# Kernel optimization log

Hardware: AMD Instinct MI355X
Metric: run time of the kernel (lower is better)

## Reference

```python
import jax, jax.numpy as jnp
import numpy as np

N_TYPES = 4
AEV_DIM = 384
HIDDEN = [160, 128, 96]
CELU_ALPHA = 0.1


def _init_params(key):
    dims = [AEV_DIM] + HIDDEN + [1]
    params = {}
    for li in range(len(dims) - 1):
        key, kw = jax.random.split(key)
        scale = 1.0 / np.sqrt(dims[li])
        # stacked over the N_TYPES per-atom-type experts
        params[f"W{li}"] = (jax.random.normal(kw, (N_TYPES, dims[li], dims[li + 1]), dtype=jnp.float32) * scale)
        params[f"b{li}"] = jnp.zeros((N_TYPES, dims[li + 1]), dtype=jnp.float32)
    return params


def setup_inputs() -> dict:
    key = jax.random.key(0)
    k1, k2, k3 = jax.random.split(key, 3)
    B, A = 2048, 64
    species = jax.random.randint(k1, (B, A), 0, N_TYPES, dtype=jnp.int64)
    aev = jax.random.normal(k2, (B, A, AEV_DIM), dtype=jnp.float32)
    inp = {"species": species, "aev": aev}
    inp.update(_init_params(k3))
    return inp


def _mlp(x, t, W0, b0, W1, b1, W2, b2, W3, b3):
    # x: [N, aev_dim] -> [N] per-atom energy for atom type t
    h = jax.nn.celu(x @ W0[t] + b0[t], alpha=CELU_ALPHA)
    h = jax.nn.celu(h @ W1[t] + b1[t], alpha=CELU_ALPHA)
    h = jax.nn.celu(h @ W2[t] + b2[t], alpha=CELU_ALPHA)
    return (h @ W3[t] + b3[t]).reshape(-1)


def reference(species, aev, W0, b0, W1, b1, W2, b2, W3, b3):
    B, A = species.shape
    sp = species.reshape(-1)            # [B*A]
    x = aev.reshape(-1, aev.shape[-1])  # [B*A, aev_dim]
    out = jnp.zeros(sp.shape, dtype=aev.dtype)  # padding_fill = 0
    for t in range(N_TYPES):  # fixed small expert set
        y = _mlp(x, t, W0, b0, W1, b1, W2, b2, W3, b3)
        out = jnp.where(sp == t, y, out)
    energies = out.reshape(B, A).sum(axis=1)  # reduce over atoms
    return species, energies
```

## Files before the change

kernel.cpp:

```cpp
#include <hip/hip_runtime.h>
#include <math.h>


#define NATOMS   131072
#define NMOL     2048
#define AEV      384
#define NTYPES   4
#define MBLK     64
#define PADTOT   (NATOMS + NTYPES * MBLK)
#define NBLK_MLP (PADTOT / MBLK)
#define NBLK_H   512

#define WB_L1 61440
#define WB_L2 81920
#define WB_T  94208

typedef __attribute__((ext_vector_type(8))) short bf16x8;
typedef __attribute__((ext_vector_type(4))) float f32x4;

__device__ __forceinline__ float celu01(float v) {
  return (v > 0.f) ? v : 0.1f * (__expf(v * 10.f) - 1.f);
}
__device__ __forceinline__ unsigned short f2bf(float x) {
  unsigned u = __float_as_uint(x);
  return (unsigned short)((u + 0x7FFFu + ((u >> 16) & 1u)) >> 16);
}
__device__ __forceinline__ float bf2f(unsigned short h) {
  return __uint_as_float(((unsigned)h) << 16);
}


__global__ void k_pre(const int* __restrict__ species, float* __restrict__ out,
                      int* __restrict__ perm, int* __restrict__ hist,
                      const float* __restrict__ W0, const float* __restrict__ W1,
                      const float* __restrict__ W2, unsigned short* __restrict__ WB) {
  const int tid = threadIdx.x, blk = blockIdx.x;
  const int i = blk * 256 + tid;
  perm[i] = -1;
  if (i < NATOMS) out[i] = (float)species[i];
  if (i < NMOL) out[NATOMS + i] = 0.f;

  for (int f = i; f < NTYPES * WB_T; f += PADTOT) {
    const int t = f / WB_T, e0 = f - t * WB_T;
    int base, NT, N;
    const float* W;
    if (e0 < WB_L1)      { base = 0;     NT = 10; N = 160; W = W0 + (size_t)t * AEV * 160; }
    else if (e0 < WB_L2) { base = WB_L1; NT = 8;  N = 128; W = W1 + (size_t)t * 160 * 128; }
    else                 { base = WB_L2; NT = 6;  N = 96;  W = W2 + (size_t)t * 128 * 96; }
    const int e = e0 - base, frag = e >> 9, r = e & 511, lane = r >> 3, j = r & 7;
    const int kt = frag / NT, nt = frag - kt * NT;
    const int k = kt * 32 + ((lane >> 4) << 3) + j, n = nt * 16 + (lane & 15);
    WB[(size_t)t * WB_T + e0] = f2bf(W[k * N + n]);
  }

  if (blk < NBLK_H) {
    const int sp = species[i];
    const int wv = tid >> 6;
    __shared__ int wc[4 * NTYPES];
#pragma unroll
    for (int t = 0; t < NTYPES; ++t) {
      const unsigned long long m = __ballot(sp == t);
      if ((tid & 63) == 0) wc[wv * NTYPES + t] = __popcll(m);
    }
    __syncthreads();
    if (tid < NTYPES)
      hist[tid * NBLK_H + blk] = wc[tid] + wc[4 + tid] + wc[8 + tid] + wc[12 + tid];
  }
}


__global__ void k_scan(const int* __restrict__ hist, int* __restrict__ poff,
                       int* __restrict__ boff) {
  __shared__ int tot[NTYPES], base[NTYPES];
  const int tid = threadIdx.x, wv = tid >> 6, lane = tid & 63;
  int s = 0;
  for (int c = 0; c < 8; ++c) s += hist[wv * NBLK_H + c * 64 + lane];
  for (int off = 32; off; off >>= 1) s += __shfl_down(s, off);
  if (lane == 0) tot[wv] = s;
  __syncthreads();
  if (tid == 0) {
    int acc = 0; poff[0] = 0;
    for (int t = 0; t < NTYPES; ++t) {
      base[t] = acc;
      acc += ((tot[t] + 63) >> 6) << 6;
      poff[t + 1] = acc;
    }
  }
  __syncthreads();
  int carry = base[wv];
  for (int c = 0; c < 8; ++c) {
    const int orig = hist[wv * NBLK_H + c * 64 + lane];
    int v = orig;
    for (int off = 1; off < 64; off <<= 1) {
      const int u = __shfl_up(v, off);
      if (lane >= off) v += u;
    }
    boff[wv * NBLK_H + c * 64 + lane] = carry + v - orig;
    carry += __shfl(v, 63);
  }
}

__global__ void k_scatter(const int* __restrict__ species, const int* __restrict__ boff,
                          int* __restrict__ perm) {
  const int tid = threadIdx.x, blk = blockIdx.x;
  const int i = blk * 256 + tid;
  const int sp = species[i];
  const int wv = tid >> 6;
  __shared__ int wc[4 * NTYPES];
  unsigned long long msel = 0;
#pragma unroll
  for (int t = 0; t < NTYPES; ++t) {
    const unsigned long long m = __ballot(sp == t);
    if ((tid & 63) == 0) wc[wv * NTYPES + t] = __popcll(m);
    if (sp == t) msel = m;
  }
  __syncthreads();
  int woff = 0;
  for (int w = 0; w < wv; ++w) woff += wc[w * NTYPES + sp];
  const int rk = __builtin_amdgcn_mbcnt_hi((unsigned)(msel >> 32),
                 __builtin_amdgcn_mbcnt_lo((unsigned)msel, 0));
  perm[boff[sp * NBLK_H + blk] + woff + rk] = i;
}


__global__ __launch_bounds__(256, 6) void k_mlp(
    const float* __restrict__ aev, const unsigned short* __restrict__ WB,
    const float* __restrict__ b0, const float* __restrict__ b1,
    const float* __restrict__ b2, const float* __restrict__ b3,
    const float* __restrict__ W3,
    const int* __restrict__ poff, const int* __restrict__ perm,
    float* __restrict__ outE)
{
  __shared__ __align__(16) unsigned short ARENA[64 * 168];
  __shared__ float red[256];
  __shared__ int   permS[64];

  const int tid  = threadIdx.x;
  const int lane = tid & 63;
  const int wv   = __builtin_amdgcn_readfirstlane(tid >> 6);
  const int quad = lane >> 4, l15 = lane & 15;
  const int slot0 = blockIdx.x * MBLK;

  if (tid < 64) permS[tid] = perm[slot0 + tid];
  int t_ = (slot0 >= poff[1]) + (slot0 >= poff[2]) + (slot0 >= poff[3]);
  if (t_ > 3) t_ = 3;
  const int t = __builtin_amdgcn_readfirstlane(t_);
  __syncthreads();

  const bf16x8* wb0 = (const bf16x8*)(WB + (size_t)t * WB_T);
  const bf16x8* wb1 = (const bf16x8*)(WB + (size_t)t * WB_T + WB_L1);
  const bf16x8* wb2 = (const bf16x8*)(WB + (size_t)t * WB_T + WB_L2);

  f32x4 acc0[10];
#pragma unroll
  for (int nt = 0; nt < 10; ++nt) {
    const float b = b0[t * 160 + nt * 16 + l15];
    acc0[nt] = (f32x4){b, b, b, b};
  }
  const int sm = tid >> 2, scg = tid & 3;
  const int sai = permS[sm];
  const float4* src = (const float4*)(aev + (size_t)(sai < 0 ? 0 : sai) * AEV);
  for (int s = 0; s < 4; ++s) {
#pragma unroll
    for (int ii = 0; ii < 6; ++ii) {
      const int c4 = scg + ii * 4;
      float4 v = make_float4(0.f, 0.f, 0.f, 0.f);
      if (sai >= 0) v = src[s * 24 + c4];
      ushort4 p = {f2bf(v.x), f2bf(v.y), f2bf(v.z), f2bf(v.w)};
      *(ushort4*)&ARENA[sm * 104 + c4 * 4] = p;
    }
    __syncthreads();
    const int arow = (wv * 16 + l15) * 104 + quad * 8;
#pragma unroll
    for (int ks = 0; ks < 3; ++ks) {
      const bf16x8 a = *(const bf16x8*)&ARENA[arow + ks * 32];
      const int ksg = s * 3 + ks;
#pragma unroll
      for (int nt = 0; nt < 10; ++nt)
        acc0[nt] = __builtin_amdgcn_mfma_f32_16x16x32_bf16(a, wb0[(ksg * 10 + nt) * 64 + lane], acc0[nt], 0, 0, 0);
    }
    __syncthreads();
  }
  {
    const int hrow0 = wv * 16 + quad * 4;
#pragma unroll
    for (int nt = 0; nt < 10; ++nt)
#pragma unroll
      for (int r = 0; r < 4; ++r)
        ARENA[(hrow0 + r) * 168 + nt * 16 + l15] = f2bf(celu01(acc0[nt][r]));
  }
  __syncthreads();

  f32x4 acc1[8];
#pragma unroll
  for (int nt = 0; nt < 8; ++nt) {
    const float b = b1[t * 128 + nt * 16 + l15];
    acc1[nt] = (f32x4){b, b, b, b};
  }
  {
    const int arow = (wv * 16 + l15) * 168 + quad * 8;
#pragma unroll
    for (int ks = 0; ks < 5; ++ks) {
      const bf16x8 a = *(const bf16x8*)&ARENA[arow + ks * 32];
#pragma unroll
      for (int nt = 0; nt < 8; ++nt)
        acc1[nt] = __builtin_amdgcn_mfma_f32_16x16x32_bf16(a, wb1[(ks * 8 + nt) * 64 + lane], acc1[nt], 0, 0, 0);
    }
  }
  __syncthreads();
  {
    const int hrow0 = wv * 16 + quad * 4;
#pragma unroll
    for (int nt = 0; nt < 8; ++nt)
#pragma unroll
      for (int r = 0; r < 4; ++r)
        ARENA[(hrow0 + r) * 136 + nt * 16 + l15] = f2bf(celu01(acc1[nt][r]));
  }
  __syncthreads();

  f32x4 acc2[6];
#pragma unroll
  for (int nt = 0; nt < 6; ++nt) {
    const float b = b2[t * 96 + nt * 16 + l15];
    acc2[nt] = (f32x4){b, b, b, b};
  }
  {
    const int arow = (wv * 16 + l15) * 136 + quad * 8;
#pragma unroll
    for (int ks = 0; ks < 4; ++ks) {
      const bf16x8 a = *(const bf16x8*)&ARENA[arow + ks * 32];
#pragma unroll
      for (int nt = 0; nt < 6; ++nt)
        acc2[nt] = __builtin_amdgcn_mfma_f32_16x16x32_bf16(a, wb2[(ks * 6 + nt) * 64 + lane], acc2[nt], 0, 0, 0);
    }
  }
  __syncthreads();
  {
    const int hrow0 = wv * 16 + quad * 4;
#pragma unroll
    for (int nt = 0; nt < 6; ++nt)
#pragma unroll
      for (int r = 0; r < 4; ++r)
        ARENA[(hrow0 + r) * 104 + nt * 16 + l15] = f2bf(celu01(acc2[nt][r]));
  }
  __syncthreads();

  const float* w3 = W3 + t * 96;
  float part = 0.f;
#pragma unroll
  for (int q = 0; q < 24; ++q) {
    const int c = wv * 24 + q;
    part = fmaf(bf2f(ARENA[lane * 104 + c]), w3[c], part);
  }
  red[wv * 64 + lane] = part;
  __syncthreads();
  if (wv == 0) {
    const float e = red[lane] + red[64 + lane] + red[128 + lane] + red[192 + lane] + b3[t];
    const int ai = permS[lane];
    if (ai >= 0) atomicAdd(&outE[ai >> 6], e);
  }
}


extern "C" void kernel_launch(void* const* d_in, const int* in_sizes, int n_in,
                              void* d_out, int out_size, void* d_ws, size_t ws_size,
                              hipStream_t stream)
{
  const int*   species = (const int*)d_in[0];
  const float* aev     = (const float*)d_in[1];
  const float* W0 = (const float*)d_in[2];
  const float* b0 = (const float*)d_in[3];
  const float* W1 = (const float*)d_in[4];
  const float* b1 = (const float*)d_in[5];
  const float* W2 = (const float*)d_in[6];
  const float* b2 = (const float*)d_in[7];
  const float* W3 = (const float*)d_in[8];
  const float* b3 = (const float*)d_in[9];
  float* out = (float*)d_out;

  int* poff = (int*)d_ws;
  int* hist = poff + 8;
  int* boff = hist + NTYPES * NBLK_H;
  int* perm = boff + NTYPES * NBLK_H;
  unsigned short* WB = (unsigned short*)(perm + PADTOT);

  k_pre    <<<PADTOT / 256, 256, 0, stream>>>(species, out, perm, hist, W0, W1, W2, WB);
  k_scan   <<<1, 256, 0, stream>>>(hist, poff, boff);
  k_scatter<<<NBLK_H, 256, 0, stream>>>(species, boff, perm);
  k_mlp    <<<NBLK_MLP, 256, 0, stream>>>(aev, WB, b0, b1, b2, b3, W3,
                                          poff, perm, out + NATOMS);
}
```

Before: 384.3 us.

## Use 2-wave blocks with two M-tiles per wave, direct AEV loads, MFMA final layer

Shrinks the MLP block to 128 threads, with each wave handling two 16-row tiles. Each weight fragment loaded from global is now reused across two MFMAs, halving weight traffic per row. The AEV input is read straight from global into registers in the MFMA A-fragment layout with software prefetch, replacing the LDS staging loop and its barriers. The last 96->1 layer becomes an MFMA instead of a scalar dot product plus LDS reduction. The cost is more accumulator registers per thread and a bf16 rounding of W3.

```diff
diff --git a/kernel.cpp b/kernel.cpp
--- a/kernel.cpp
+++ b/kernel.cpp
@@ -25,8 +25,11 @@
   unsigned u = __float_as_uint(x);
   return (unsigned short)((u + 0x7FFFu + ((u >> 16) & 1u)) >> 16);
 }
-__device__ __forceinline__ float bf2f(unsigned short h) {
-  return __uint_as_float(((unsigned)h) << 16);
+__device__ __forceinline__ unsigned int pk2(float lo, float hi) {
+  unsigned a = __float_as_uint(lo), b = __float_as_uint(hi);
+  a = (a + 0x7FFFu + ((a >> 16) & 1u)) >> 16;
+  b = ((b + 0x7FFFu + ((b >> 16) & 1u)) >> 16) << 16;
+  return a | b;
 }
 
 
@@ -123,7 +126,7 @@
 }
 
 
-__global__ __launch_bounds__(256, 6) void k_mlp(
+__global__ __launch_bounds__(128) void k_mlp(
     const float* __restrict__ aev, const unsigned short* __restrict__ WB,
     const float* __restrict__ b0, const float* __restrict__ b1,
     const float* __restrict__ b2, const float* __restrict__ b3,
@@ -131,9 +134,8 @@
     const int* __restrict__ poff, const int* __restrict__ perm,
     float* __restrict__ outE)
 {
-  __shared__ __align__(16) unsigned short ARENA[64 * 168];
-  __shared__ float red[256];
-  __shared__ int   permS[64];
+  __shared__ __align__(16) unsigned short H[64 * 168];
+  __shared__ int permS[64];
 
   const int tid  = threadIdx.x;
   const int lane = tid & 63;
@@ -147,118 +149,164 @@
   const int t = __builtin_amdgcn_readfirstlane(t_);
   __syncthreads();
 
+  const float* rp[2];
+#pragma unroll
+  for (int mtl = 0; mtl < 2; ++mtl) {
+    const int ai = permS[(2 * wv + mtl) * 16 + l15];
+    rp[mtl] = aev + (size_t)(ai < 0 ? 0 : ai) * AEV + quad * 8;
+  }
+
   const bf16x8* wb0 = (const bf16x8*)(WB + (size_t)t * WB_T);
   const bf16x8* wb1 = (const bf16x8*)(WB + (size_t)t * WB_T + WB_L1);
   const bf16x8* wb2 = (const bf16x8*)(WB + (size_t)t * WB_T + WB_L2);
 
-  f32x4 acc0[10];
+  union U8 { unsigned int u[4]; bf16x8 v; };
+
+  f32x4 acc0[10][2];
 #pragma unroll
   for (int nt = 0; nt < 10; ++nt) {
     const float b = b0[t * 160 + nt * 16 + l15];
-    acc0[nt] = (f32x4){b, b, b, b};
-  }
-  const int sm = tid >> 2, scg = tid & 3;
-  const int sai = permS[sm];
-  const float4* src = (const float4*)(aev + (size_t)(sai < 0 ? 0 : sai) * AEV);
-  for (int s = 0; s < 4; ++s) {
-#pragma unroll
-    for (int ii = 0; ii < 6; ++ii) {
-      const int c4 = scg + ii * 4;
-      float4 v = make_float4(0.f, 0.f, 0.f, 0.f);
-      if (sai >= 0) v = src[s * 24 + c4];
-      ushort4 p = {f2bf(v.x), f2bf(v.y), f2bf(v.z), f2bf(v.w)};
-      *(ushort4*)&ARENA[sm * 104 + c4 * 4] = p;
-    }
-    __syncthreads();
-    const int arow = (wv * 16 + l15) * 104 + quad * 8;
-#pragma unroll
-    for (int ks = 0; ks < 3; ++ks) {
-      const bf16x8 a = *(const bf16x8*)&ARENA[arow + ks * 32];
-      const int ksg = s * 3 + ks;
-#pragma unroll
-      for (int nt = 0; nt < 10; ++nt)
-        acc0[nt] = __builtin_amdgcn_mfma_f32_16x16x32_bf16(a, wb0[(ksg * 10 + nt) * 64 + lane], acc0[nt], 0, 0, 0);
-    }
-    __syncthreads();
-  }
-  {
-    const int hrow0 = wv * 16 + quad * 4;
-#pragma unroll
-    for (int nt = 0; nt < 10; ++nt)
+#pragma unroll
+    for (int mtl = 0; mtl < 2; ++mtl) acc0[nt][mtl] = (f32x4){b, b, b, b};
+  }
+
+  float4 raw[2][2];
+#pragma unroll
+  for (int mtl = 0; mtl < 2; ++mtl) {
+    raw[mtl][0] = *(const float4*)(rp[mtl]);
+    raw[mtl][1] = *(const float4*)(rp[mtl] + 4);
+  }
+
+  for (int ks = 0; ks < 12; ++ks) {
+    bf16x8 a[2];
+#pragma unroll
+    for (int mtl = 0; mtl < 2; ++mtl) {
+      U8 c;
+      c.u[0] = pk2(raw[mtl][0].x, raw[mtl][0].y);
+      c.u[1] = pk2(raw[mtl][0].z, raw[mtl][0].w);
+      c.u[2] = pk2(raw[mtl][1].x, raw[mtl][1].y);
+      c.u[3] = pk2(raw[mtl][1].z, raw[mtl][1].w);
+      a[mtl] = c.v;
+    }
+    if (ks < 11) {
+#pragma unroll
+      for (int mtl = 0; mtl < 2; ++mtl) {
+        const float* p = rp[mtl] + (ks + 1) * 32;
+        raw[mtl][0] = *(const float4*)p;
+        raw[mtl][1] = *(const float4*)(p + 4);
+      }
+    }
+#pragma unroll
+    for (int nt = 0; nt < 10; ++nt) {
+      const bf16x8 w = wb0[(ks * 10 + nt) * 64 + lane];
+#pragma unroll
+      for (int mtl = 0; mtl < 2; ++mtl)
+        acc0[nt][mtl] = __builtin_amdgcn_mfma_f32_16x16x32_bf16(a[mtl], w, acc0[nt][mtl], 0, 0, 0);
+    }
+  }
+#pragma unroll
+  for (int nt = 0; nt < 10; ++nt)
+#pragma unroll
+    for (int mtl = 0; mtl < 2; ++mtl)
 #pragma unroll
       for (int r = 0; r < 4; ++r)
-        ARENA[(hrow0 + r) * 168 + nt * 16 + l15] = f2bf(celu01(acc0[nt][r]));
-  }
-  __syncthreads();
-
-  f32x4 acc1[8];
+        H[((2 * wv + mtl) * 16 + quad * 4 + r) * 168 + nt * 16 + l15] = f2bf(celu01(acc0[nt][mtl][r]));
+  __syncthreads();
+
+  f32x4 acc1[8][2];
 #pragma unroll
   for (int nt = 0; nt < 8; ++nt) {
     const float b = b1[t * 128 + nt * 16 + l15];
-    acc1[nt] = (f32x4){b, b, b, b};
-  }
-  {
-    const int arow = (wv * 16 + l15) * 168 + quad * 8;
-#pragma unroll
-    for (int ks = 0; ks < 5; ++ks) {
-      const bf16x8 a = *(const bf16x8*)&ARENA[arow + ks * 32];
-#pragma unroll
-      for (int nt = 0; nt < 8; ++nt)
-        acc1[nt] = __builtin_amdgcn_mfma_f32_16x16x32_bf16(a, wb1[(ks * 8 + nt) * 64 + lane], acc1[nt], 0, 0, 0);
-    }
-  }
-  __syncthreads();
-  {
-    const int hrow0 = wv * 16 + quad * 4;
-#pragma unroll
-    for (int nt = 0; nt < 8; ++nt)
+#pragma unroll
+    for (int mtl = 0; mtl < 2; ++mtl) acc1[nt][mtl] = (f32x4){b, b, b, b};
+  }
+#pragma unroll
+  for (int ks = 0; ks < 5; ++ks) {
+    bf16x8 a[2];
+#pragma unroll
+    for (int mtl = 0; mtl < 2; ++mtl)
+      a[mtl] = *(const bf16x8*)&H[((2 * wv + mtl) * 16 + l15) * 168 + quad * 8 + ks * 32];
+#pragma unroll
+    for (int nt = 0; nt < 8; ++nt) {
+      const bf16x8 w = wb1[(ks * 8 + nt) * 64 + lane];
+#pragma unroll
+      for (int mtl = 0; mtl < 2; ++mtl)
+        acc1[nt][mtl] = __builtin_amdgcn_mfma_f32_16x16x32_bf16(a[mtl], w, acc1[nt][mtl], 0, 0, 0);
+    }
+  }
+  __syncthreads();
+#pragma unroll
+  for (int nt = 0; nt < 8; ++nt)
+#pragma unroll
+    for (int mtl = 0; mtl < 2; ++mtl)
 #pragma unroll
       for (int r = 0; r < 4; ++r)
-        ARENA[(hrow0 + r) * 136 + nt * 16 + l15] = f2bf(celu01(acc1[nt][r]));
-  }
-  __syncthreads();
-
-  f32x4 acc2[6];
+        H[((2 * wv + mtl) * 16 + quad * 4 + r) * 136 + nt * 16 + l15] = f2bf(celu01(acc1[nt][mtl][r]));
+  __syncthreads();
+
+  f32x4 acc2[6][2];
 #pragma unroll
   for (int nt = 0; nt < 6; ++nt) {
     const float b = b2[t * 96 + nt * 16 + l15];
-    acc2[nt] = (f32x4){b, b, b, b};
-  }
-  {
-    const int arow = (wv * 16 + l15) * 136 + quad * 8;
-#pragma unroll
-    for (int ks = 0; ks < 4; ++ks) {
-      const bf16x8 a = *(const bf16x8*)&ARENA[arow + ks * 32];
-#pragma unroll
-      for (int nt = 0; nt < 6; ++nt)
-        acc2[nt] = __builtin_amdgcn_mfma_f32_16x16x32_bf16(a, wb2[(ks * 6 + nt) * 64 + lane], acc2[nt], 0, 0, 0);
-    }
-  }
-  __syncthreads();
-  {
-    const int hrow0 = wv * 16 + quad * 4;
-#pragma unroll
-    for (int nt = 0; nt < 6; ++nt)
+#pragma unroll
+    for (int mtl = 0; mtl < 2; ++mtl) acc2[nt][mtl] = (f32x4){b, b, b, b};
+  }
+#pragma unroll
+  for (int ks = 0; ks < 4; ++ks) {
+    bf16x8 a[2];
+#pragma unroll
+    for (int mtl = 0; mtl < 2; ++mtl)
+      a[mtl] = *(const bf16x8*)&H[((2 * wv + mtl) * 16 + l15) * 136 + quad * 8 + ks * 32];
+#pragma unroll
+    for (int nt = 0; nt < 6; ++nt) {
+      const bf16x8 w = wb2[(ks * 6 + nt) * 64 + lane];
+#pragma unroll
+      for (int mtl = 0; mtl < 2; ++mtl)
+        acc2[nt][mtl] = __builtin_amdgcn_mfma_f32_16x16x32_bf16(a[mtl], w, acc2[nt][mtl], 0, 0, 0);
+    }
+  }
+  __syncthreads();
+#pragma unroll
+  for (int nt = 0; nt < 6; ++nt)
+#pragma unroll
+    for (int mtl = 0; mtl < 2; ++mtl)
 #pragma unroll
       for (int r = 0; r < 4; ++r)
-        ARENA[(hrow0 + r) * 104 + nt * 16 + l15] = f2bf(celu01(acc2[nt][r]));
-  }
-  __syncthreads();
-
-  const float* w3 = W3 + t * 96;
-  float part = 0.f;
-#pragma unroll
-  for (int q = 0; q < 24; ++q) {
-    const int c = wv * 24 + q;
-    part = fmaf(bf2f(ARENA[lane * 104 + c]), w3[c], part);
-  }
-  red[wv * 64 + lane] = part;
-  __syncthreads();
-  if (wv == 0) {
-    const float e = red[lane] + red[64 + lane] + red[128 + lane] + red[192 + lane] + b3[t];
-    const int ai = permS[lane];
-    if (ai >= 0) atomicAdd(&outE[ai >> 6], e);
-  }
+        H[((2 * wv + mtl) * 16 + quad * 4 + r) * 104 + nt * 16 + l15] = f2bf(celu01(acc2[nt][mtl][r]));
+  __syncthreads();
+
+  bf16x8 w3f[3];
+#pragma unroll
+  for (int ks = 0; ks < 3; ++ks) {
+    const float* wp = W3 + t * 96 + ks * 32 + quad * 8;
+    const float4 f0 = *(const float4*)wp;
+    const float4 f1 = *(const float4*)(wp + 4);
+    U8 c;
+    c.u[0] = pk2(f0.x, f0.y);
+    c.u[1] = pk2(f0.z, f0.w);
+    c.u[2] = pk2(f1.x, f1.y);
+    c.u[3] = pk2(f1.z, f1.w);
+    w3f[ks] = c.v;
+  }
+  f32x4 accE[2];
+#pragma unroll
+  for (int mtl = 0; mtl < 2; ++mtl) accE[mtl] = (f32x4){0.f, 0.f, 0.f, 0.f};
+#pragma unroll
+  for (int mtl = 0; mtl < 2; ++mtl)
+#pragma unroll
+    for (int ks = 0; ks < 3; ++ks) {
+      const bf16x8 a = *(const bf16x8*)&H[((2 * wv + mtl) * 16 + l15) * 104 + quad * 8 + ks * 32];
+      accE[mtl] = __builtin_amdgcn_mfma_f32_16x16x32_bf16(a, w3f[ks], accE[mtl], 0, 0, 0);
+    }
+  const float bb3 = b3[t];
+#pragma unroll
+  for (int mtl = 0; mtl < 2; ++mtl)
+#pragma unroll
+    for (int r = 0; r < 4; ++r)
+      if (l15 == 0) {
+        const int ai = permS[(2 * wv + mtl) * 16 + quad * 4 + r];
+        if (ai >= 0) atomicAdd(&outE[ai >> 6], accE[mtl][r] + bb3);
+      }
 }
 
 
@@ -287,6 +335,6 @@
   k_pre    <<<PADTOT / 256, 256, 0, stream>>>(species, out, perm, hist, W0, W1, W2, WB);
   k_scan   <<<1, 256, 0, stream>>>(hist, poff, boff);
   k_scatter<<<NBLK_H, 256, 0, stream>>>(species, boff, perm);
-  k_mlp    <<<NBLK_MLP, 256, 0, stream>>>(aev, WB, b0, b1, b2, b3, W3,
+  k_mlp    <<<NBLK_MLP, 128, 0, stream>>>(aev, WB, b0, b1, b2, b3, W3,
                                           poff, perm, out + NATOMS);
 }
```

New measurement: 360.2 us. 6.3% less time.
